# Kernel optimization log

Hardware: AMD Instinct MI355X
Metric: run time of the kernel (lower is better)

Reference implementation:

```python
import jax, jax.numpy as jnp
import numpy as np

B, S, DM, TD, H, HD = 2, 2048, 1024, 1024, 16, 64


def setup_inputs() -> dict:
    key = jax.random.key(0)
    k1, k2, k3, k4 = jax.random.split(key, 4)
    query = jax.random.normal(k1, (B, S, DM), dtype=jnp.float32)
    # fused QKV projection weight (nn.Linear weight layout: [out, in]) and output proj
    W_in = jax.random.normal(k2, (3 * TD, DM), dtype=jnp.float32) * 0.02
    W_out = jax.random.normal(k3, (DM, TD), dtype=jnp.float32) * 0.02
    # standard RoPE tables, broadcastable against [B, H, S, HD]
    inv_freq = 1.0 / (10000.0 ** (jnp.arange(0, HD, 2, dtype=jnp.float32) / HD))
    t = jnp.arange(S, dtype=jnp.float32)
    freqs = jnp.outer(t, inv_freq)                      # [S, HD/2]
    emb = jnp.concatenate([freqs, freqs], axis=-1)      # [S, HD]
    sin_q = jnp.sin(emb)[None, None]                    # [1,1,S,HD]
    cos_q = jnp.cos(emb)[None, None]
    # padding mask over keys: first length[b] positions valid (>= S/2 so no NaN rows)
    lengths = jax.random.randint(k4, (B,), S // 2, S + 1)
    attn_mask = jnp.arange(S)[None, :] < lengths[:, None]  # [B, S] bool
    return {"query": query, "W_in": W_in, "W_out": W_out,
            "sin_q": sin_q, "cos_q": cos_q, "attn_mask": attn_mask}


def _rotate_half(x):
    x1, x2 = jnp.split(x, 2, axis=-1)
    return jnp.concatenate([-x2, x1], axis=-1)


def reference(query, W_in, W_out, sin_q, cos_q, attn_mask):
    # fused QKV projection (proj_in, bias=False)
    qkv = query @ W_in.T                                # [B, S, 3*TD]
    q, k, v = jnp.split(qkv, 3, axis=-1)
    to_heads = lambda x: x.reshape(B, S, H, HD).transpose(0, 2, 1, 3)  # [B,H,S,HD]
    q, k, v = to_heads(q), to_heads(k), to_heads(v)
    # RoPE (prefix = 0 since sin covers full sequence)
    q = q * cos_q + _rotate_half(q) * sin_q
    k = k * cos_q + _rotate_half(k) * sin_q
    # SDPA with padding-mask bias + causal mask
    scale = 1.0 / jnp.sqrt(jnp.float32(HD))
    scores = jnp.einsum('bhqd,bhkd->bhqk', q, k) * scale  # [B,H,S,S]
    causal = jnp.arange(S)[:, None] >= jnp.arange(S)[None, :]  # [S, S]
    mask = attn_mask[:, None, None, :] & causal[None, None]    # [B,1,S,S]
    scores = jnp.where(mask, scores, -jnp.inf)
    attn = jax.nn.softmax(scores, axis=-1)
    out = jnp.einsum('bhqk,bhkd->bhqd', attn, v)        # [B,H,S,HD]
    out = out.transpose(0, 2, 1, 3).reshape(B, S, TD)
    return out @ W_out.T                                 # [B, S, DM]
```

## Files before the change

### kernel.cpp

```cpp
#include <hip/hip_runtime.h>
#include <hip/hip_bf16.h>

#define B_ 2
#define S_ 2048
#define DM_ 1024
#define TD_ 1024
#define H_ 16
#define HD_ 64

using bf16 = __hip_bfloat16;
typedef __attribute__((ext_vector_type(8))) short s8v;
typedef __attribute__((ext_vector_type(4))) float f4v;

__device__ __forceinline__ f4v mfma_bf16(s8v a, s8v b, f4v c) {
    return __builtin_amdgcn_mfma_f32_16x16x32_bf16(a, b, c, 0, 0, 0);
}

__device__ __forceinline__ unsigned cvt_pk_bf16(float a, float b) {
    unsigned r;
    asm("v_cvt_pk_bf16_f32 %0, %1, %2" : "=v"(r) : "v"(a), "v"(b));
    return r;
}
__device__ __forceinline__ int2 pack4bf(float a, float b, float c, float d) {
    int2 r;
    r.x = (int)cvt_pk_bf16(a, b);
    r.y = (int)cvt_pk_bf16(c, d);
    return r;
}

__device__ __forceinline__ bool detect_f32(const unsigned int* __restrict__ cosw) {
    return (cosw[0] & 0xFFFFu) == 0u;
}

__device__ __forceinline__ float ld_f(const void* p, int idx, bool f32) {
    return f32 ? ((const float*)p)[idx]
               : __bfloat162float(((const bf16*)p)[idx]);
}

__device__ __forceinline__ void gload_lds16(const bf16* g, void* l) {
    __builtin_amdgcn_global_load_lds(
        (const __attribute__((address_space(1))) unsigned int*)(const void*)g,
        (__attribute__((address_space(3))) unsigned int*)l,
        16, 0, 0);
}

#define NQ_  (B_ * S_ * DM_)
#define NWI_ (3 * TD_ * DM_)
#define NWO_ (DM_ * TD_)
__global__ __launch_bounds__(256)
void cvt_all(const void* __restrict__ q, const void* __restrict__ wi,
             const void* __restrict__ wo, bf16* __restrict__ dst,
             const unsigned int* __restrict__ cosw) {
    const bool f32 = detect_f32(cosw);
    int i = (blockIdx.x * 256 + threadIdx.x) * 8;
    const void* src; int off;
    if (i < NQ_)              { src = q;  off = i; }
    else if (i < NQ_ + NWI_)  { src = wi; off = i - NQ_; }
    else                      { src = wo; off = i - NQ_ - NWI_; }
    if (f32) {
        const float* p = (const float*)src + off;
        float4 x = *reinterpret_cast<const float4*>(p);
        float4 y = *reinterpret_cast<const float4*>(p + 4);
        union { unsigned u[4]; int4 v; } t;
        t.u[0] = cvt_pk_bf16(x.x, x.y);
        t.u[1] = cvt_pk_bf16(x.z, x.w);
        t.u[2] = cvt_pk_bf16(y.x, y.y);
        t.u[3] = cvt_pk_bf16(y.z, y.w);
        *reinterpret_cast<int4*>(dst + i) = t.v;
    } else {
        *reinterpret_cast<int4*>(dst + i) =
            *reinterpret_cast<const int4*>((const bf16*)src + off);
    }
}

__global__ __launch_bounds__(256)
void compute_lengths(const void* __restrict__ mask, int* __restrict__ lengths) {
    int b = blockIdx.x;
    unsigned int w0 = ((const unsigned int*)mask)[0];
    int enc;
    if (w0 == 1u) enc = 0;
    else if (w0 == 0x01010101u) enc = 1;
    else if (w0 == 0x3F803F80u) enc = 2;
    else enc = 3;
    int cnt = 0;
    for (int s = threadIdx.x; s < S_; s += 256) {
        int i = b * S_ + s;
        bool v;
        if (enc == 0)      v = ((const int*)mask)[i] != 0;
        else if (enc == 1) v = ((const unsigned char*)mask)[i] != 0;
        else if (enc == 2) v = ((const unsigned short*)mask)[i] != 0;
        else               v = ((const float*)mask)[i] != 0.f;
        cnt += v ? 1 : 0;
    }
    __shared__ int red[256];
    red[threadIdx.x] = cnt;
    __syncthreads();
    for (int off = 128; off > 0; off >>= 1) {
        if (threadIdx.x < off) red[threadIdx.x] += red[threadIdx.x + off];
        __syncthreads();
    }
    if (threadIdx.x == 0) lengths[b] = red[0];
}

__global__ __launch_bounds__(256)
void gemm_nt(const bf16* __restrict__ A, const bf16* __restrict__ Bm,
             void* __restrict__ C, int M, int N, int K,
             int c_dyn, const unsigned int* __restrict__ cosw) {
    __shared__ bf16 lds_a[128 * 64];
    __shared__ bf16 lds_b[128 * 64];

    const bool cf32 = c_dyn && detect_f32(cosw);

    const int t = threadIdx.x;
    const int wave = t >> 6, lane = t & 63;
    const int quad = lane >> 4, l16 = lane & 15;
    const int wm = wave >> 1, wn = wave & 1;
    const int m0 = blockIdx.y * 128, n0 = blockIdx.x * 128;
    const int wuni = __builtin_amdgcn_readfirstlane(wave);

    f4v acc[4][4];
    #pragma unroll
    for (int i = 0; i < 4; i++)
        #pragma unroll
        for (int j = 0; j < 4; j++)
            acc[i][j] = f4v{0.f, 0.f, 0.f, 0.f};

    for (int k0 = 0; k0 < K; k0 += 64) {
        __syncthreads();
        #pragma unroll
        for (int i = 0; i < 4; i++) {
            int ci = i * 256 + t;
            int row = ci >> 3;
            int csrc = (ci & 7) ^ (row & 7);
            gload_lds16(A + (size_t)(m0 + row) * K + k0 + csrc * 8,
                        (char*)lds_a + i * 4096 + wuni * 1024);
            gload_lds16(Bm + (size_t)(n0 + row) * K + k0 + csrc * 8,
                        (char*)lds_b + i * 4096 + wuni * 1024);
        }
        __syncthreads();

        #pragma unroll
        for (int kk = 0; kk < 2; kk++) {
            s8v afr[4], bfr[4];
            #pragma unroll
            for (int mb = 0; mb < 4; mb++) {
                int r = wm * 64 + mb * 16 + l16;
                int ch = (kk * 4 + quad) ^ (l16 & 7);
                afr[mb] = *reinterpret_cast<const s8v*>(&lds_a[r * 64 + ch * 8]);
            }
            #pragma unroll
            for (int nb = 0; nb < 4; nb++) {
                int r = wn * 64 + nb * 16 + l16;
                int ch = (kk * 4 + quad) ^ (l16 & 7);
                bfr[nb] = *reinterpret_cast<const s8v*>(&lds_b[r * 64 + ch * 8]);
            }
            #pragma unroll
            for (int mb = 0; mb < 4; mb++)
                #pragma unroll
                for (int nb = 0; nb < 4; nb++)
                    acc[mb][nb] = mfma_bf16(bfr[nb], afr[mb], acc[mb][nb]);
        }
    }

    #pragma unroll
    for (int mb = 0; mb < 4; mb++) {
        int m = m0 + wm * 64 + mb * 16 + l16;
        #pragma unroll
        for (int nb = 0; nb < 4; nb++) {
            int n = n0 + wn * 64 + nb * 16 + quad * 4;
            f4v v = acc[mb][nb];
            if (cf32) {
                *reinterpret_cast<f4v*>(&((float*)C)[(size_t)m * N + n]) = v;
            } else {
                *reinterpret_cast<int2*>(&((bf16*)C)[(size_t)m * N + n]) =
                    pack4bf(v[0], v[1], v[2], v[3]);
            }
        }
    }
}

__global__ __launch_bounds__(256)
void rope_split(const bf16* __restrict__ qkv,
                const void* __restrict__ sin_t, const void* __restrict__ cos_t,
                bf16* __restrict__ Qh, bf16* __restrict__ Kt) {
    const bool f32 = detect_f32((const unsigned int*)cos_t);
    int idx = blockIdx.x * 256 + threadIdx.x;
    int d = idx & 63;
    int h = (idx >> 6) & 15;
    int s = (idx >> 10) & 2047;
    int b = idx >> 21;
    size_t row = (size_t)(b * S_ + s) * 3072;
    int col  = h * 64 + d;
    int colp = h * 64 + ((d + 32) & 63);
    float sgn = (d < 32) ? -1.f : 1.f;
    float cs = ld_f(cos_t, s * 64 + d, f32);
    float sn = ld_f(sin_t, s * 64 + d, f32);
    float q  = __bfloat162float(qkv[row + col]);
    float qp = __bfloat162float(qkv[row + colp]);
    float k  = __bfloat162float(qkv[row + 1024 + col]);
    float kp = __bfloat162float(qkv[row + 1024 + colp]);
    Qh[((size_t)((b * H_ + h) * S_ + s)) * 64 + d] =
        __float2bfloat16((q * cs + sgn * qp * sn) * 0.180336880f);
    size_t ktile = ((size_t)(b * H_ + h) * 32 + (s >> 6)) * 4096;
    int dp = ((((d >> 3) ^ (s & 7)) << 3) | (d & 7));
    Kt[ktile + (s & 63) * 64 + dp] = __float2bfloat16(k * cs + sgn * kp * sn);
}

__global__ __launch_bounds__(256)
void v_transpose(const bf16* __restrict__ qkv, bf16* __restrict__ Vt) {
    __shared__ bf16 tile[64 * 72];
    const int t = threadIdx.x;
    const int sb = blockIdx.x, h = blockIdx.y, b = blockIdx.z;
    #pragma unroll
    for (int i = 0; i < 2; i++) {
        int id = i * 256 + t;
        int row = id >> 3, c = id & 7;
        *reinterpret_cast<int4*>(&tile[row * 72 + c * 8]) =
            *reinterpret_cast<const int4*>(
                qkv + (size_t)(b * S_ + sb * 64 + row) * 3072 + 2048 + h * 64 + c * 8);
    }
    __syncthreads();
    const size_t tb = ((size_t)(b * H_ + h) * 32 + sb) * 4096;
    #pragma unroll
    for (int i = 0; i < 2; i++) {
        int id = i * 256 + t;
        int d = id >> 3, kc = id & 7;
        union { short s[8]; int4 v; } u;
        #pragma unroll
        for (int e = 0; e < 8; e++)
            u.s[e] = reinterpret_cast<const short*>(tile)[(kc * 8 + e) * 72 + d];
        *reinterpret_cast<int4*>(Vt + tb + d * 64 + ((kc ^ (d & 7)) * 8)) = u.v;
    }
}

__global__ __launch_bounds__(256)
void attn_fused(const bf16* __restrict__ Qh, const bf16* __restrict__ Kt,
                const bf16* __restrict__ Vt, const int* __restrict__ lengths,
                bf16* __restrict__ out) {
    __shared__ bf16 k_buf[2 * 4096];
    __shared__ bf16 v_buf[2 * 4096];
    __shared__ bf16 lds_p[4 * 16 * 72];

    const int t = threadIdx.x, wave = t >> 6, lane = t & 63;
    const int quad = lane >> 4, l16 = lane & 15;
    const int bid = blockIdx.x;
    const int slot = bid >> 3;
    const int bh = (bid & 7) * 4 + (slot >> 5);
    const int qb = slot & 31;
    const int b = bh >> 4, h = bh & 15;

    const size_t hb = (size_t)bh * S_ * 64;
    const bf16* Ktp = Kt + (size_t)bh * 32 * 4096;
    const bf16* Vtp = Vt + (size_t)bh * 32 * 4096;
    const int wuni = __builtin_amdgcn_readfirstlane(wave);
    int len_raw = lengths[b];
    const int len_b = len_raw < 1 ? 1 : (len_raw > S_ ? S_ : len_raw);

    const int qbase = qb * 64;
    const int qrow_g = qbase + wave * 16 + l16;
    const int kmax = (qrow_g < len_b - 1) ? qrow_g : (len_b - 1);

    s8v qf[2];
    {
        const bf16* qptr = Qh + hb + (size_t)qrow_g * 64 + quad * 8;
        qf[0] = *reinterpret_cast<const s8v*>(qptr);
        qf[1] = *reinterpret_cast<const s8v*>(qptr + 32);
    }

    f4v o_acc[4];
    #pragma unroll
    for (int a = 0; a < 4; a++) o_acc[a] = f4v{0.f, 0.f, 0.f, 0.f};
    float l_sum = 0.f;

    const int nkt_len = (len_b + 63) >> 6;
    const int nkt = (qb + 1) < nkt_len ? (qb + 1) : nkt_len;

    f4v s_prev[4];
    auto process_tile = [&](int pt, const bf16* vb) {
        const int pbase = pt * 64;
        const bool tail = (pt == qb) || (pbase + 64 > len_b);
        #pragma unroll
        for (int a = 0; a < 4; a++) {
            float e0[4];
            #pragma unroll
            for (int r = 0; r < 4; r++) {
                float e = __builtin_amdgcn_exp2f(s_prev[a][r]);
                if (tail) {
                    int key = pbase + a * 16 + quad * 4 + r;
                    e = (key <= kmax) ? e : 0.f;
                }
                e0[r] = e;
                l_sum += e;
            }
            *reinterpret_cast<int2*>(
                &lds_p[(wave * 16 + l16) * 72 + a * 16 + quad * 4]) =
                pack4bf(e0[0], e0[1], e0[2], e0[3]);
        }
        asm volatile("s_waitcnt lgkmcnt(0)" ::: "memory");
        #pragma unroll
        for (int kk = 0; kk < 2; kk++) {
            s8v pf = *reinterpret_cast<const s8v*>(
                &lds_p[(wave * 16 + l16) * 72 + kk * 32 + quad * 8]);
            #pragma unroll
            for (int a = 0; a < 4; a++) {
                int ch = (kk * 4 + quad) ^ (l16 & 7);
                s8v vf = *reinterpret_cast<const s8v*>(
                    &vb[(a * 16 + l16) * 64 + ch * 8]);
                o_acc[a] = mfma_bf16(vf, pf, o_acc[a]);
            }
        }
    };

    #pragma unroll
    for (int i = 0; i < 2; i++) {
        int ci = i * 256 + t;
        gload_lds16(Ktp + ci * 8, (char*)k_buf + i * 4096 + wuni * 1024);
    }
    __syncthreads();

    for (int kt = 0; kt < nkt; kt++) {
        const int cur = kt & 1;
        {
            const bf16* vst = Vtp + (size_t)kt * 4096;
            #pragma unroll
            for (int i = 0; i < 2; i++) {
                int ci = i * 256 + t;
                gload_lds16(vst + ci * 8,
                            (char*)v_buf + cur * 8192 + i * 4096 + wuni * 1024);
            }
        }
        if (kt + 1 < nkt) {
            const bf16* kst = Ktp + (size_t)(kt + 1) * 4096;
            #pragma unroll
            for (int i = 0; i < 2; i++) {
                int ci = i * 256 + t;
                gload_lds16(kst + ci * 8,
                            (char*)k_buf + (cur ^ 1) * 8192 + i * 4096 + wuni * 1024);
            }
        }

        const bf16* kb = k_buf + cur * 4096;
        f4v s_acc[4];
        #pragma unroll
        for (int a = 0; a < 4; a++) s_acc[a] = f4v{0.f, 0.f, 0.f, 0.f};
        #pragma unroll
        for (int kk = 0; kk < 2; kk++) {
            #pragma unroll
            for (int a = 0; a < 4; a++) {
                int ch = (kk * 4 + quad) ^ (l16 & 7);
                s8v kf = *reinterpret_cast<const s8v*>(
                    &kb[(a * 16 + l16) * 64 + ch * 8]);
                s_acc[a] = mfma_bf16(kf, qf[kk], s_acc[a]);
            }
        }

        if (kt > 0) process_tile(kt - 1, v_buf + ((kt - 1) & 1) * 4096);

        #pragma unroll
        for (int a = 0; a < 4; a++) s_prev[a] = s_acc[a];

        __syncthreads();
    }
    process_tile(nkt - 1, v_buf + ((nkt - 1) & 1) * 4096);

    l_sum += __shfl_xor(l_sum, 16);
    l_sum += __shfl_xor(l_sum, 32);
    float inv_l = 1.f / l_sum;
    size_t orow = ((size_t)(b * S_ + qrow_g)) * TD_ + h * 64;
    #pragma unroll
    for (int a = 0; a < 4; a++) {
        *reinterpret_cast<int2*>(&out[orow + a * 16 + quad * 4]) =
            pack4bf(o_acc[a][0] * inv_l, o_acc[a][1] * inv_l,
                    o_acc[a][2] * inv_l, o_acc[a][3] * inv_l);
    }
}

extern "C" void kernel_launch(void* const* d_in, const int* in_sizes, int n_in,
                              void* d_out, int out_size, void* d_ws, size_t ws_size,
                              hipStream_t stream) {
    const void* query = d_in[0];
    const void* W_in  = d_in[1];
    const void* W_out = d_in[2];
    const void* sin_q = d_in[3];
    const void* cos_q = d_in[4];
    const void* mask  = d_in[5];
    const unsigned int* cosw = (const unsigned int*)cos_q;

    const size_t nQ  = NQ_;
    const size_t nWi = NWI_;
    const size_t nWo = NWO_;

    bf16* qkv  = (bf16*)d_ws;
    bf16* Qh   = qkv + (size_t)4096 * 3072;
    bf16* Kt   = Qh + nQ;
    bf16* qbf  = Kt + nQ;
    bf16* wibf = qbf + nQ;
    bf16* wobf = wibf + nWi;
    int* lengths = (int*)(wobf + nWo);
    bf16* Vt   = qbf;
    bf16* attn = qkv;

    compute_lengths<<<B_, 256, 0, stream>>>(mask, lengths);
    cvt_all<<<(int)((nQ + nWi + nWo) / (256 * 8)), 256, 0, stream>>>(
        query, W_in, W_out, qbf, cosw);

    dim3 g1(3072 / 128, 4096 / 128);
    gemm_nt<<<g1, 256, 0, stream>>>(qbf, wibf, qkv, 4096, 3072, 1024, 0, cosw);

    rope_split<<<(B_ * S_ * H_ * HD_) / 256, 256, 0, stream>>>(qkv, sin_q, cos_q, Qh, Kt);
    dim3 gv(S_ / 64, H_, B_);
    v_transpose<<<gv, 256, 0, stream>>>(qkv, Vt);

    attn_fused<<<1024, 256, 0, stream>>>(Qh, Kt, Vt, lengths, attn);

    dim3 g2(1024 / 128, 4096 / 128);
    gemm_nt<<<g2, 256, 0, stream>>>(attn, wobf, d_out, 4096, 1024, 1024, 1, cosw);
}
```

Baseline: 206.8 us.

## Pair causal query blocks per attention block and merge small prep kernels

The attention kernel now launches 512 blocks, and each one processes two query blocks (p and 31-p) in sequence. This balances the triangular causal workload across blocks. The length computation is merged into the conversion kernel, and rope and V transpose are merged into one launch, which removes launch overhead. The trade-offs are fewer resident attention blocks (512 rather than 1024) with a longer serial chain per block, and the K/V tiles are reloaded for the second pass.

Measured after the change: 193.3 us. -6.5%, faster.

```diff
diff --git a/kernel.cpp b/kernel.cpp
--- a/kernel.cpp
+++ b/kernel.cpp
@@ -47,35 +47,38 @@
 #define NQ_  (B_ * S_ * DM_)
 #define NWI_ (3 * TD_ * DM_)
 #define NWO_ (DM_ * TD_)
+#define NCVT_BLOCKS ((NQ_ + NWI_ + NWO_) / 2048)
+
 __global__ __launch_bounds__(256)
-void cvt_all(const void* __restrict__ q, const void* __restrict__ wi,
-             const void* __restrict__ wo, bf16* __restrict__ dst,
-             const unsigned int* __restrict__ cosw) {
-    const bool f32 = detect_f32(cosw);
-    int i = (blockIdx.x * 256 + threadIdx.x) * 8;
-    const void* src; int off;
-    if (i < NQ_)              { src = q;  off = i; }
-    else if (i < NQ_ + NWI_)  { src = wi; off = i - NQ_; }
-    else                      { src = wo; off = i - NQ_ - NWI_; }
-    if (f32) {
-        const float* p = (const float*)src + off;
-        float4 x = *reinterpret_cast<const float4*>(p);
-        float4 y = *reinterpret_cast<const float4*>(p + 4);
-        union { unsigned u[4]; int4 v; } t;
-        t.u[0] = cvt_pk_bf16(x.x, x.y);
-        t.u[1] = cvt_pk_bf16(x.z, x.w);
-        t.u[2] = cvt_pk_bf16(y.x, y.y);
-        t.u[3] = cvt_pk_bf16(y.z, y.w);
-        *reinterpret_cast<int4*>(dst + i) = t.v;
-    } else {
-        *reinterpret_cast<int4*>(dst + i) =
-            *reinterpret_cast<const int4*>((const bf16*)src + off);
-    }
-}
-
-__global__ __launch_bounds__(256)
-void compute_lengths(const void* __restrict__ mask, int* __restrict__ lengths) {
-    int b = blockIdx.x;
+void prep_all(const void* __restrict__ q, const void* __restrict__ wi,
+              const void* __restrict__ wo, bf16* __restrict__ dst,
+              const void* __restrict__ mask, int* __restrict__ lengths,
+              const unsigned int* __restrict__ cosw) {
+    const int bid = blockIdx.x;
+    if (bid < NCVT_BLOCKS) {
+        const bool f32 = detect_f32(cosw);
+        int i = (bid * 256 + threadIdx.x) * 8;
+        const void* src; int off;
+        if (i < NQ_)              { src = q;  off = i; }
+        else if (i < NQ_ + NWI_)  { src = wi; off = i - NQ_; }
+        else                      { src = wo; off = i - NQ_ - NWI_; }
+        if (f32) {
+            const float* p = (const float*)src + off;
+            float4 x = *reinterpret_cast<const float4*>(p);
+            float4 y = *reinterpret_cast<const float4*>(p + 4);
+            union { unsigned u[4]; int4 v; } t;
+            t.u[0] = cvt_pk_bf16(x.x, x.y);
+            t.u[1] = cvt_pk_bf16(x.z, x.w);
+            t.u[2] = cvt_pk_bf16(y.x, y.y);
+            t.u[3] = cvt_pk_bf16(y.z, y.w);
+            *reinterpret_cast<int4*>(dst + i) = t.v;
+        } else {
+            *reinterpret_cast<int4*>(dst + i) =
+                *reinterpret_cast<const int4*>((const bf16*)src + off);
+        }
+        return;
+    }
+    int b = bid - NCVT_BLOCKS;
     unsigned int w0 = ((const unsigned int*)mask)[0];
     int enc;
     if (w0 == 1u) enc = 0;
@@ -180,37 +183,38 @@
 }
 
 __global__ __launch_bounds__(256)
-void rope_split(const bf16* __restrict__ qkv,
-                const void* __restrict__ sin_t, const void* __restrict__ cos_t,
-                bf16* __restrict__ Qh, bf16* __restrict__ Kt) {
-    const bool f32 = detect_f32((const unsigned int*)cos_t);
-    int idx = blockIdx.x * 256 + threadIdx.x;
-    int d = idx & 63;
-    int h = (idx >> 6) & 15;
-    int s = (idx >> 10) & 2047;
-    int b = idx >> 21;
-    size_t row = (size_t)(b * S_ + s) * 3072;
-    int col  = h * 64 + d;
-    int colp = h * 64 + ((d + 32) & 63);
-    float sgn = (d < 32) ? -1.f : 1.f;
-    float cs = ld_f(cos_t, s * 64 + d, f32);
-    float sn = ld_f(sin_t, s * 64 + d, f32);
-    float q  = __bfloat162float(qkv[row + col]);
-    float qp = __bfloat162float(qkv[row + colp]);
-    float k  = __bfloat162float(qkv[row + 1024 + col]);
-    float kp = __bfloat162float(qkv[row + 1024 + colp]);
-    Qh[((size_t)((b * H_ + h) * S_ + s)) * 64 + d] =
-        __float2bfloat16((q * cs + sgn * qp * sn) * 0.180336880f);
-    size_t ktile = ((size_t)(b * H_ + h) * 32 + (s >> 6)) * 4096;
-    int dp = ((((d >> 3) ^ (s & 7)) << 3) | (d & 7));
-    Kt[ktile + (s & 63) * 64 + dp] = __float2bfloat16(k * cs + sgn * kp * sn);
-}
-
-__global__ __launch_bounds__(256)
-void v_transpose(const bf16* __restrict__ qkv, bf16* __restrict__ Vt) {
+void rope_vt(const bf16* __restrict__ qkv,
+             const void* __restrict__ sin_t, const void* __restrict__ cos_t,
+             bf16* __restrict__ Qh, bf16* __restrict__ Kt, bf16* __restrict__ Vt) {
     __shared__ bf16 tile[64 * 72];
+    const int bid = blockIdx.x;
+    if (bid < 16384) {
+        const bool f32 = detect_f32((const unsigned int*)cos_t);
+        int idx = bid * 256 + threadIdx.x;
+        int d = idx & 63;
+        int h = (idx >> 6) & 15;
+        int s = (idx >> 10) & 2047;
+        int b = idx >> 21;
+        size_t row = (size_t)(b * S_ + s) * 3072;
+        int col  = h * 64 + d;
+        int colp = h * 64 + ((d + 32) & 63);
+        float sgn = (d < 32) ? -1.f : 1.f;
+        float cs = ld_f(cos_t, s * 64 + d, f32);
+        float sn = ld_f(sin_t, s * 64 + d, f32);
+        float q  = __bfloat162float(qkv[row + col]);
+        float qp = __bfloat162float(qkv[row + colp]);
+        float k  = __bfloat162float(qkv[row + 1024 + col]);
+        float kp = __bfloat162float(qkv[row + 1024 + colp]);
+        Qh[((size_t)((b * H_ + h) * S_ + s)) * 64 + d] =
+            __float2bfloat16((q * cs + sgn * qp * sn) * 0.180336880f);
+        size_t ktile = ((size_t)(b * H_ + h) * 32 + (s >> 6)) * 4096;
+        int dp = ((((d >> 3) ^ (s & 7)) << 3) | (d & 7));
+        Kt[ktile + (s & 63) * 64 + dp] = __float2bfloat16(k * cs + sgn * kp * sn);
+        return;
+    }
+    const int vid = bid - 16384;
+    const int sb = vid & 31, h = (vid >> 5) & 15, b = vid >> 9;
     const int t = threadIdx.x;
-    const int sb = blockIdx.x, h = blockIdx.y, b = blockIdx.z;
     #pragma unroll
     for (int i = 0; i < 2; i++) {
         int id = i * 256 + t;
@@ -245,8 +249,8 @@
     const int quad = lane >> 4, l16 = lane & 15;
     const int bid = blockIdx.x;
     const int slot = bid >> 3;
-    const int bh = (bid & 7) * 4 + (slot >> 5);
-    const int qb = slot & 31;
+    const int bh = (bid & 7) * 4 + (slot >> 4);
+    const int p = slot & 15;
     const int b = bh >> 4, h = bh & 15;
 
     const size_t hb = (size_t)bh * S_ * 64;
@@ -255,123 +259,127 @@
     const int wuni = __builtin_amdgcn_readfirstlane(wave);
     int len_raw = lengths[b];
     const int len_b = len_raw < 1 ? 1 : (len_raw > S_ ? S_ : len_raw);
-
-    const int qbase = qb * 64;
-    const int qrow_g = qbase + wave * 16 + l16;
-    const int kmax = (qrow_g < len_b - 1) ? qrow_g : (len_b - 1);
-
-    s8v qf[2];
-    {
-        const bf16* qptr = Qh + hb + (size_t)qrow_g * 64 + quad * 8;
-        qf[0] = *reinterpret_cast<const s8v*>(qptr);
-        qf[1] = *reinterpret_cast<const s8v*>(qptr + 32);
-    }
-
-    f4v o_acc[4];
+    const int nkt_len = (len_b + 63) >> 6;
+
     #pragma unroll
-    for (int a = 0; a < 4; a++) o_acc[a] = f4v{0.f, 0.f, 0.f, 0.f};
-    float l_sum = 0.f;
-
-    const int nkt_len = (len_b + 63) >> 6;
-    const int nkt = (qb + 1) < nkt_len ? (qb + 1) : nkt_len;
-
-    f4v s_prev[4];
-    auto process_tile = [&](int pt, const bf16* vb) {
-        const int pbase = pt * 64;
-        const bool tail = (pt == qb) || (pbase + 64 > len_b);
+    for (int pass = 0; pass < 2; pass++) {
+        const int qb = pass ? (31 - p) : p;
+        const int qbase = qb * 64;
+        const int qrow_g = qbase + wave * 16 + l16;
+        const int kmax = (qrow_g < len_b - 1) ? qrow_g : (len_b - 1);
+
+        s8v qf[2];
+        {
+            const bf16* qptr = Qh + hb + (size_t)qrow_g * 64 + quad * 8;
+            qf[0] = *reinterpret_cast<const s8v*>(qptr);
+            qf[1] = *reinterpret_cast<const s8v*>(qptr + 32);
+        }
+
+        f4v o_acc[4];
+        #pragma unroll
+        for (int a = 0; a < 4; a++) o_acc[a] = f4v{0.f, 0.f, 0.f, 0.f};
+        float l_sum = 0.f;
+
+        const int nkt = (qb + 1) < nkt_len ? (qb + 1) : nkt_len;
+
+        f4v s_prev[4];
+        auto process_tile = [&](int pt, const bf16* vb) {
+            const int pbase = pt * 64;
+            const bool tail = (pt == qb) || (pbase + 64 > len_b);
+            #pragma unroll
+            for (int a = 0; a < 4; a++) {
+                float e0[4];
+                #pragma unroll
+                for (int r = 0; r < 4; r++) {
+                    float e = __builtin_amdgcn_exp2f(s_prev[a][r]);
+                    if (tail) {
+                        int key = pbase + a * 16 + quad * 4 + r;
+                        e = (key <= kmax) ? e : 0.f;
+                    }
+                    e0[r] = e;
+                    l_sum += e;
+                }
+                *reinterpret_cast<int2*>(
+                    &lds_p[(wave * 16 + l16) * 72 + a * 16 + quad * 4]) =
+                    pack4bf(e0[0], e0[1], e0[2], e0[3]);
+            }
+            asm volatile("s_waitcnt lgkmcnt(0)" ::: "memory");
+            #pragma unroll
+            for (int kk = 0; kk < 2; kk++) {
+                s8v pf = *reinterpret_cast<const s8v*>(
+                    &lds_p[(wave * 16 + l16) * 72 + kk * 32 + quad * 8]);
+                #pragma unroll
+                for (int a = 0; a < 4; a++) {
+                    int ch = (kk * 4 + quad) ^ (l16 & 7);
+                    s8v vf = *reinterpret_cast<const s8v*>(
+                        &vb[(a * 16 + l16) * 64 + ch * 8]);
+                    o_acc[a] = mfma_bf16(vf, pf, o_acc[a]);
+                }
+            }
+        };
+
+        #pragma unroll
+        for (int i = 0; i < 2; i++) {
+            int ci = i * 256 + t;
+            gload_lds16(Ktp + ci * 8, (char*)k_buf + i * 4096 + wuni * 1024);
+        }
+        __syncthreads();
+
+        for (int kt = 0; kt < nkt; kt++) {
+            const int cur = kt & 1;
+            {
+                const bf16* vst = Vtp + (size_t)kt * 4096;
+                #pragma unroll
+                for (int i = 0; i < 2; i++) {
+                    int ci = i * 256 + t;
+                    gload_lds16(vst + ci * 8,
+                                (char*)v_buf + cur * 8192 + i * 4096 + wuni * 1024);
+                }
+            }
+            if (kt + 1 < nkt) {
+                const bf16* kst = Ktp + (size_t)(kt + 1) * 4096;
+                #pragma unroll
+                for (int i = 0; i < 2; i++) {
+                    int ci = i * 256 + t;
+                    gload_lds16(kst + ci * 8,
+                                (char*)k_buf + (cur ^ 1) * 8192 + i * 4096 + wuni * 1024);
+                }
+            }
+
+            const bf16* kb = k_buf + cur * 4096;
+            f4v s_acc[4];
+            #pragma unroll
+            for (int a = 0; a < 4; a++) s_acc[a] = f4v{0.f, 0.f, 0.f, 0.f};
+            #pragma unroll
+            for (int kk = 0; kk < 2; kk++) {
+                #pragma unroll
+                for (int a = 0; a < 4; a++) {
+                    int ch = (kk * 4 + quad) ^ (l16 & 7);
+                    s8v kf = *reinterpret_cast<const s8v*>(
+                        &kb[(a * 16 + l16) * 64 + ch * 8]);
+                    s_acc[a] = mfma_bf16(kf, qf[kk], s_acc[a]);
+                }
+            }
+
+            if (kt > 0) process_tile(kt - 1, v_buf + ((kt - 1) & 1) * 4096);
+
+            #pragma unroll
+            for (int a = 0; a < 4; a++) s_prev[a] = s_acc[a];
+
+            __syncthreads();
+        }
+        process_tile(nkt - 1, v_buf + ((nkt - 1) & 1) * 4096);
+
+        l_sum += __shfl_xor(l_sum, 16);
+        l_sum += __shfl_xor(l_sum, 32);
+        float inv_l = 1.f / l_sum;
+        size_t orow = ((size_t)(b * S_ + qrow_g)) * TD_ + h * 64;
         #pragma unroll
         for (int a = 0; a < 4; a++) {
-            float e0[4];
-            #pragma unroll
-            for (int r = 0; r < 4; r++) {
-                float e = __builtin_amdgcn_exp2f(s_prev[a][r]);
-                if (tail) {
-                    int key = pbase + a * 16 + quad * 4 + r;
-                    e = (key <= kmax) ? e : 0.f;
-                }
-                e0[r] = e;
-                l_sum += e;
-            }
-            *reinterpret_cast<int2*>(
-                &lds_p[(wave * 16 + l16) * 72 + a * 16 + quad * 4]) =
-                pack4bf(e0[0], e0[1], e0[2], e0[3]);
-        }
-        asm volatile("s_waitcnt lgkmcnt(0)" ::: "memory");
-        #pragma unroll
-        for (int kk = 0; kk < 2; kk++) {
-            s8v pf = *reinterpret_cast<const s8v*>(
-                &lds_p[(wave * 16 + l16) * 72 + kk * 32 + quad * 8]);
-            #pragma unroll
-            for (int a = 0; a < 4; a++) {
-                int ch = (kk * 4 + quad) ^ (l16 & 7);
-                s8v vf = *reinterpret_cast<const s8v*>(
-                    &vb[(a * 16 + l16) * 64 + ch * 8]);
-                o_acc[a] = mfma_bf16(vf, pf, o_acc[a]);
-            }
-        }
-    };
-
-    #pragma unroll
-    for (int i = 0; i < 2; i++) {
-        int ci = i * 256 + t;
-        gload_lds16(Ktp + ci * 8, (char*)k_buf + i * 4096 + wuni * 1024);
-    }
-    __syncthreads();
-
-    for (int kt = 0; kt < nkt; kt++) {
-        const int cur = kt & 1;
-        {
-            const bf16* vst = Vtp + (size_t)kt * 4096;
-            #pragma unroll
-            for (int i = 0; i < 2; i++) {
-                int ci = i * 256 + t;
-                gload_lds16(vst + ci * 8,
-                            (char*)v_buf + cur * 8192 + i * 4096 + wuni * 1024);
-            }
-        }
-        if (kt + 1 < nkt) {
-            const bf16* kst = Ktp + (size_t)(kt + 1) * 4096;
-            #pragma unroll
-            for (int i = 0; i < 2; i++) {
-                int ci = i * 256 + t;
-                gload_lds16(kst + ci * 8,
-                            (char*)k_buf + (cur ^ 1) * 8192 + i * 4096 + wuni * 1024);
-            }
-        }
-
-        const bf16* kb = k_buf + cur * 4096;
-        f4v s_acc[4];
-        #pragma unroll
-        for (int a = 0; a < 4; a++) s_acc[a] = f4v{0.f, 0.f, 0.f, 0.f};
-        #pragma unroll
-        for (int kk = 0; kk < 2; kk++) {
-            #pragma unroll
-            for (int a = 0; a < 4; a++) {
-                int ch = (kk * 4 + quad) ^ (l16 & 7);
-                s8v kf = *reinterpret_cast<const s8v*>(
-                    &kb[(a * 16 + l16) * 64 + ch * 8]);
-                s_acc[a] = mfma_bf16(kf, qf[kk], s_acc[a]);
-            }
-        }
-
-        if (kt > 0) process_tile(kt - 1, v_buf + ((kt - 1) & 1) * 4096);
-
-        #pragma unroll
-        for (int a = 0; a < 4; a++) s_prev[a] = s_acc[a];
-
-        __syncthreads();
-    }
-    process_tile(nkt - 1, v_buf + ((nkt - 1) & 1) * 4096);
-
-    l_sum += __shfl_xor(l_sum, 16);
-    l_sum += __shfl_xor(l_sum, 32);
-    float inv_l = 1.f / l_sum;
-    size_t orow = ((size_t)(b * S_ + qrow_g)) * TD_ + h * 64;
-    #pragma unroll
-    for (int a = 0; a < 4; a++) {
-        *reinterpret_cast<int2*>(&out[orow + a * 16 + quad * 4]) =
-            pack4bf(o_acc[a][0] * inv_l, o_acc[a][1] * inv_l,
-                    o_acc[a][2] * inv_l, o_acc[a][3] * inv_l);
+            *reinterpret_cast<int2*>(&out[orow + a * 16 + quad * 4]) =
+                pack4bf(o_acc[a][0] * inv_l, o_acc[a][1] * inv_l,
+                        o_acc[a][2] * inv_l, o_acc[a][3] * inv_l);
+        }
     }
 }
 
@@ -400,18 +408,15 @@
     bf16* Vt   = qbf;
     bf16* attn = qkv;
 
-    compute_lengths<<<B_, 256, 0, stream>>>(mask, lengths);
-    cvt_all<<<(int)((nQ + nWi + nWo) / (256 * 8)), 256, 0, stream>>>(
-        query, W_in, W_out, qbf, cosw);
+    prep_all<<<NCVT_BLOCKS + B_, 256, 0, stream>>>(
+        query, W_in, W_out, qbf, mask, lengths, cosw);
 
     dim3 g1(3072 / 128, 4096 / 128);
     gemm_nt<<<g1, 256, 0, stream>>>(qbf, wibf, qkv, 4096, 3072, 1024, 0, cosw);
 
-    rope_split<<<(B_ * S_ * H_ * HD_) / 256, 256, 0, stream>>>(qkv, sin_q, cos_q, Qh, Kt);
-    dim3 gv(S_ / 64, H_, B_);
-    v_transpose<<<gv, 256, 0, stream>>>(qkv, Vt);
-
-    attn_fused<<<1024, 256, 0, stream>>>(Qh, Kt, Vt, lengths, attn);
+    rope_vt<<<16384 + 1024, 256, 0, stream>>>(qkv, sin_q, cos_q, Qh, Kt, Vt);
+
+    attn_fused<<<512, 256, 0, stream>>>(Qh, Kt, Vt, lengths, attn);
 
     dim3 g2(1024 / 128, 4096 / 128);
     gemm_nt<<<g2, 256, 0, stream>>>(attn, wobf, d_out, 4096, 1024, 1024, 1, cosw);
```
